# Kernel optimization log

Measured on AMD Instinct MI355X. Metric: run time of the kernel, lower is better.

Reference implementation:

```python
import jax, jax.numpy as jnp
import numpy as np

N1, N2, C, H = 512, 512, 256, 512

def setup_inputs() -> dict:
    key = jax.random.key(0)
    ks = jax.random.split(key, 8)
    std = 0.01
    return {
        "X": jax.random.normal(ks[0], (N1, C), dtype=jnp.float32),
        "Y": jax.random.normal(ks[1], (N2, C), dtype=jnp.float32),
        "W_sr": jax.random.normal(ks[2], (C, C), dtype=jnp.float32) * std,   # project_sr.weight
        "W_tg": jax.random.normal(ks[3], (C, C), dtype=jnp.float32) * std,   # project_tg.weight
        "W1": jax.random.normal(ks[4], (H, 2 * C), dtype=jnp.float32) * std, # fc_M[0].weight [512,512]
        "b1": jnp.zeros((H,), dtype=jnp.float32),                            # fc_M[0].bias
        "w2": jax.random.normal(ks[5], (1, H), dtype=jnp.float32) * std,     # fc_M[2].weight [1,512]
        "b2": jnp.zeros((1,), dtype=jnp.float32),                            # fc_M[2].bias
    }

def reference(X, Y, W_sr, W_tg, W1, b1, w2, b2):
    # Projections (Linear without bias): x @ W.T
    Xp = X @ W_sr.T  # [N1, C]
    Yp = Y @ W_tg.T  # [N2, C]
    # fc_M first layer acts on concat([X_k, Y_k], -1); split W1 into the
    # halves that multiply Xp and Yp respectively (mathematically identical
    # to materializing the [N1,N2,2C] concat, but avoids it).
    W1x, W1y = W1[:, :C], W1[:, C:]
    hx = Xp @ W1x.T                     # [N1, H]
    hy = Yp @ W1y.T                     # [N2, H]
    Hid = jax.nn.relu(hx[:, None, :] + hy[None, :, :] + b1)  # [N1, N2, H]
    M = Hid @ w2[0] + b2[0]             # [N1, N2]  (squeeze of last dim 1)
    return M
```

## Files before the change

### kernel.cpp

```cpp
#include <hip/hip_runtime.h>


typedef _Float16 h2 __attribute__((ext_vector_type(2)));
typedef _Float16 h4 __attribute__((ext_vector_type(4)));
typedef _Float16 h8 __attribute__((ext_vector_type(8)));

__global__ __launch_bounds__(128) void gemm1_f16(
    const float* __restrict__ A0, const float* __restrict__ A1,
    const float* __restrict__ B0, const float* __restrict__ B1,
    _Float16* __restrict__ C0, _Float16* __restrict__ C1,
    const float* __restrict__ b2, float* __restrict__ out)
{
    const int z = blockIdx.z;
    const float* A = z ? A1 : A0;
    const float* B = z ? B1 : B0;
    _Float16* Cc   = z ? C1 : C0;

    __shared__ _Float16 As2[16 * 72];
    __shared__ _Float16 Bs2[16 * 72];

    const int t  = threadIdx.x;
    const int m0 = blockIdx.x * 32;
    const int n0 = blockIdx.y * 32;
    const int ti = t >> 4;
    const int tj = t & 15;

    {
        const int bid = blockIdx.x + 16 * (blockIdx.y + 8 * blockIdx.z);
        const float bb = b2[0];
        float4 f = {bb, bb, bb, bb};
        float* o = out + bid * 1024 + t * 8;
        *(float4*)o = f;
        *(float4*)(o + 4) = f;
    }

    float acc[4][2] = {};

    float4 va[2], vb[2];
    #pragma unroll
    for (int r = 0; r < 2; r++) {
        const int id = t + r * 128;
        va[r] = *(const float4*)&A[(m0 + (id >> 3)) * 256 + (id & 7) * 4];
        vb[r] = *(const float4*)&B[(n0 + (id >> 3)) * 256 + (id & 7) * 4];
    }

    for (int kt = 0; kt < 256; kt += 32) {
        #pragma unroll
        for (int r = 0; r < 2; r++) {
            const int id  = t + r * 128;
            const int m   = id >> 3;
            const int k4  = (id & 7) * 4;
            const int kp0 = k4 >> 1;
            h2 alo = {(_Float16)va[r].x, (_Float16)va[r].y};
            h2 ahi = {(_Float16)va[r].z, (_Float16)va[r].w};
            *(h2*)&As2[kp0 * 72 + 2 * m]       = alo;
            *(h2*)&As2[(kp0 + 1) * 72 + 2 * m] = ahi;
            h2 blo = {(_Float16)vb[r].x, (_Float16)vb[r].y};
            h2 bhi = {(_Float16)vb[r].z, (_Float16)vb[r].w};
            *(h2*)&Bs2[kp0 * 72 + 2 * m]       = blo;
            *(h2*)&Bs2[(kp0 + 1) * 72 + 2 * m] = bhi;
        }
        __syncthreads();

        if (kt < 224) {
            #pragma unroll
            for (int r = 0; r < 2; r++) {
                const int id = t + r * 128;
                va[r] = *(const float4*)&A[(m0 + (id >> 3)) * 256 + kt + 32 + (id & 7) * 4];
                vb[r] = *(const float4*)&B[(n0 + (id >> 3)) * 256 + kt + 32 + (id & 7) * 4];
            }
        }

        #pragma unroll 8
        for (int kp = 0; kp < 16; kp++) {
            h8 a = *(const h8*)&As2[kp * 72 + 8 * ti];
            h4 b = *(const h4*)&Bs2[kp * 72 + 4 * tj];
            const h2* ap = (const h2*)&a;
            const h2* bp = (const h2*)&b;
            #pragma unroll
            for (int mi = 0; mi < 4; mi++)
                #pragma unroll
                for (int nj = 0; nj < 2; nj++)
                    acc[mi][nj] = __builtin_amdgcn_fdot2(ap[mi], bp[nj],
                                                         acc[mi][nj], false);
        }
        __syncthreads();
    }

    #pragma unroll
    for (int mi = 0; mi < 4; mi++) {
        const int m = m0 + 4 * ti + mi;
        h2 r = {(_Float16)acc[mi][0], (_Float16)acc[mi][1]};
        *(h2*)&Cc[m * 256 + n0 + 2 * tj] = r;
    }
}

__global__ __launch_bounds__(128) void gemm2_f16(
    const _Float16* __restrict__ A0, const _Float16* __restrict__ A1,
    const float* __restrict__ B0, const float* __restrict__ B1,
    _Float16* __restrict__ C0, _Float16* __restrict__ C1,
    const float* __restrict__ bias1)
{
    const int z = blockIdx.z;
    const _Float16* A = z ? A1 : A0;
    const float* B    = z ? B1 : B0;
    _Float16* Cc      = z ? C1 : C0;
    const float* bias = z ? bias1 : nullptr;

    __shared__ _Float16 As2[16 * 72];
    __shared__ _Float16 Bs2[16 * 136];

    const int t  = threadIdx.x;
    const int m0 = blockIdx.x * 32;
    const int n0 = blockIdx.y * 64;
    const int ti = t >> 4;
    const int tj = t & 15;

    float acc[4][4] = {};

    h8 va;
    float4 vb[4];
    {
        const int m  = t >> 2;
        const int k8 = (t & 3) * 8;
        va = *(const h8*)&A[(m0 + m) * 256 + k8];
    }
    #pragma unroll
    for (int r = 0; r < 4; r++) {
        const int id = t + r * 128;
        vb[r] = *(const float4*)&B[(n0 + (id >> 3)) * 512 + (id & 7) * 4];
    }

    for (int kt = 0; kt < 256; kt += 32) {
        {
            const int m   = t >> 2;
            const int k8  = (t & 3) * 8;
            const int kp0 = k8 >> 1;
            #pragma unroll
            for (int i = 0; i < 4; i++) {
                h2 p = {va[2 * i], va[2 * i + 1]};
                *(h2*)&As2[(kp0 + i) * 72 + 2 * m] = p;
            }
        }
        #pragma unroll
        for (int r = 0; r < 4; r++) {
            const int id  = t + r * 128;
            const int n   = id >> 3;
            const int k4  = (id & 7) * 4;
            const int kp0 = k4 >> 1;
            h2 lo = {(_Float16)vb[r].x, (_Float16)vb[r].y};
            h2 hi = {(_Float16)vb[r].z, (_Float16)vb[r].w};
            *(h2*)&Bs2[kp0 * 136 + 2 * n]       = lo;
            *(h2*)&Bs2[(kp0 + 1) * 136 + 2 * n] = hi;
        }
        __syncthreads();

        if (kt < 224) {
            const int m  = t >> 2;
            const int k8 = (t & 3) * 8;
            va = *(const h8*)&A[(m0 + m) * 256 + kt + 32 + k8];
            #pragma unroll
            for (int r = 0; r < 4; r++) {
                const int id = t + r * 128;
                vb[r] = *(const float4*)&B[(n0 + (id >> 3)) * 512 + kt + 32 + (id & 7) * 4];
            }
        }

        #pragma unroll 8
        for (int kp = 0; kp < 16; kp++) {
            h8 a = *(const h8*)&As2[kp * 72 + 8 * ti];
            h8 b = *(const h8*)&Bs2[kp * 136 + 8 * tj];
            const h2* ap = (const h2*)&a;
            const h2* bp = (const h2*)&b;
            #pragma unroll
            for (int mi = 0; mi < 4; mi++)
                #pragma unroll
                for (int nj = 0; nj < 4; nj++)
                    acc[mi][nj] = __builtin_amdgcn_fdot2(ap[mi], bp[nj],
                                                         acc[mi][nj], false);
        }
        __syncthreads();
    }

    float4 bv = {0.f, 0.f, 0.f, 0.f};
    if (bias) bv = *(const float4*)&bias[n0 + 4 * tj];
    #pragma unroll
    for (int mi = 0; mi < 4; mi++) {
        const int m = m0 + 4 * ti + mi;
        h4 r = {(_Float16)(acc[mi][0] + bv.x), (_Float16)(acc[mi][1] + bv.y),
                (_Float16)(acc[mi][2] + bv.z), (_Float16)(acc[mi][3] + bv.w)};
        *(h4*)&Cc[m * 512 + n0 + 4 * tj] = r;
    }
}

__global__ __launch_bounds__(256) void affinity_core(
    const _Float16* __restrict__ hx, const _Float16* __restrict__ hy,
    const float* __restrict__ w2, float* __restrict__ out)
{
    __shared__ __align__(16) _Float16 xs[64 * 72];
    __shared__ __align__(16) _Float16 ys[64 * 72];
    __shared__ __align__(16) _Float16 ws2[64];

    const int t  = threadIdx.x;
    const int i0 = blockIdx.x * 64;
    const int j0 = blockIdx.y * 64;
    const int h0 = blockIdx.z * 64;
    const int ti = t / 16;
    const int tj = t % 16;

    #pragma unroll
    for (int s = 0; s < 2; s++) {
        const int id = t + s * 256;
        const int r  = id >> 3;
        const int c8 = (id & 7) * 8;
        *(float4*)&xs[r * 72 + c8] = *(const float4*)&hx[(i0 + r) * 512 + h0 + c8];
        *(float4*)&ys[r * 72 + c8] = *(const float4*)&hy[(j0 + r) * 512 + h0 + c8];
    }
    if (t < 64) ws2[t] = (_Float16)w2[h0 + t];
    __syncthreads();

    float acc[4][4] = {};
    const _Float16* xr = xs + ti * 72;
    const _Float16* yr = ys + tj * 72;
    const h2 hz = {(_Float16)0.f, (_Float16)0.f};

    #pragma unroll 2
    for (int g = 0; g < 8; g++) {
        const int ho = g * 8;
        h8 w = *(const h8*)&ws2[ho];
        h8 x[4], y[4];
        #pragma unroll
        for (int m = 0; m < 4; m++) x[m] = *(const h8*)&xr[m * (16 * 72) + ho];
        #pragma unroll
        for (int n = 0; n < 4; n++) y[n] = *(const h8*)&yr[n * (16 * 72) + ho];
        const h2* wp = (const h2*)&w;
        #pragma unroll
        for (int m = 0; m < 4; m++) {
            const h2* xp = (const h2*)&x[m];
            #pragma unroll
            for (int n = 0; n < 4; n++) {
                const h2* yp = (const h2*)&y[n];
                float a = acc[m][n];
                #pragma unroll
                for (int p = 0; p < 4; p++) {
                    h2 s = xp[p] + yp[p];
                    s = __builtin_elementwise_max(s, hz);
                    a = __builtin_amdgcn_fdot2(s, wp[p], a, false);
                }
                acc[m][n] = a;
            }
        }
    }

    #pragma unroll
    for (int m = 0; m < 4; m++) {
        #pragma unroll
        for (int n = 0; n < 4; n++) {
            atomicAdd(&out[(i0 + ti + 16 * m) * 512 + (j0 + tj + 16 * n)],
                      acc[m][n]);
        }
    }
}

extern "C" void kernel_launch(void* const* d_in, const int* in_sizes, int n_in,
                              void* d_out, int out_size, void* d_ws, size_t ws_size,
                              hipStream_t stream) {
    const float* X    = (const float*)d_in[0];
    const float* Y    = (const float*)d_in[1];
    const float* W_sr = (const float*)d_in[2];
    const float* W_tg = (const float*)d_in[3];
    const float* W1   = (const float*)d_in[4];
    const float* b1   = (const float*)d_in[5];
    const float* w2   = (const float*)d_in[6];
    const float* b2   = (const float*)d_in[7];

    float* ws = (float*)d_ws;
    _Float16* Xp = (_Float16*)ws;
    _Float16* Yp = (_Float16*)(ws + 65536);
    _Float16* hx = (_Float16*)(ws + 131072);
    _Float16* hy = (_Float16*)(ws + 262144);
    float* out = (float*)d_out;

    gemm1_f16<<<dim3(16, 8, 2), 128, 0, stream>>>(
        X, Y, W_sr, W_tg, Xp, Yp, b2, out);
    gemm2_f16<<<dim3(16, 8, 2), 128, 0, stream>>>(
        Xp, Yp, W1, W1 + 256, hx, hy, b1);
    affinity_core<<<dim3(8, 8, 8), 256, 0, stream>>>(hx, hy, w2, out);
}
```

Baseline: 98.58 us.

## Load full K panel into shared memory once in both projection GEMMs

```diff
diff --git a/kernel.cpp b/kernel.cpp
--- a/kernel.cpp
+++ b/kernel.cpp
@@ -16,8 +16,8 @@
     const float* B = z ? B1 : B0;
     _Float16* Cc   = z ? C1 : C0;
 
-    __shared__ _Float16 As2[16 * 72];
-    __shared__ _Float16 Bs2[16 * 72];
+    __shared__ _Float16 As2[128 * 72];
+    __shared__ _Float16 Bs2[128 * 72];
 
     const int t  = threadIdx.x;
     const int m0 = blockIdx.x * 32;
@@ -34,57 +34,42 @@
         *(float4*)(o + 4) = f;
     }
 
-    float acc[4][2] = {};
-
-    float4 va[2], vb[2];
-    #pragma unroll
-    for (int r = 0; r < 2; r++) {
-        const int id = t + r * 128;
-        va[r] = *(const float4*)&A[(m0 + (id >> 3)) * 256 + (id & 7) * 4];
-        vb[r] = *(const float4*)&B[(n0 + (id >> 3)) * 256 + (id & 7) * 4];
-    }
-
-    for (int kt = 0; kt < 256; kt += 32) {
-        #pragma unroll
-        for (int r = 0; r < 2; r++) {
-            const int id  = t + r * 128;
+    #pragma unroll 4
+    for (int r = 0; r < 8; r++) {
+        const int kt = r * 32;
+        #pragma unroll
+        for (int s = 0; s < 2; s++) {
+            const int id  = t + s * 128;
             const int m   = id >> 3;
             const int k4  = (id & 7) * 4;
-            const int kp0 = k4 >> 1;
-            h2 alo = {(_Float16)va[r].x, (_Float16)va[r].y};
-            h2 ahi = {(_Float16)va[r].z, (_Float16)va[r].w};
+            const int kp0 = r * 16 + (k4 >> 1);
+            float4 va = *(const float4*)&A[(m0 + m) * 256 + kt + k4];
+            h2 alo = {(_Float16)va.x, (_Float16)va.y};
+            h2 ahi = {(_Float16)va.z, (_Float16)va.w};
             *(h2*)&As2[kp0 * 72 + 2 * m]       = alo;
             *(h2*)&As2[(kp0 + 1) * 72 + 2 * m] = ahi;
-            h2 blo = {(_Float16)vb[r].x, (_Float16)vb[r].y};
-            h2 bhi = {(_Float16)vb[r].z, (_Float16)vb[r].w};
+            float4 vb = *(const float4*)&B[(n0 + m) * 256 + kt + k4];
+            h2 blo = {(_Float16)vb.x, (_Float16)vb.y};
+            h2 bhi = {(_Float16)vb.z, (_Float16)vb.w};
             *(h2*)&Bs2[kp0 * 72 + 2 * m]       = blo;
             *(h2*)&Bs2[(kp0 + 1) * 72 + 2 * m] = bhi;
         }
-        __syncthreads();
-
-        if (kt < 224) {
-            #pragma unroll
-            for (int r = 0; r < 2; r++) {
-                const int id = t + r * 128;
-                va[r] = *(const float4*)&A[(m0 + (id >> 3)) * 256 + kt + 32 + (id & 7) * 4];
-                vb[r] = *(const float4*)&B[(n0 + (id >> 3)) * 256 + kt + 32 + (id & 7) * 4];
-            }
-        }
-
-        #pragma unroll 8
-        for (int kp = 0; kp < 16; kp++) {
-            h8 a = *(const h8*)&As2[kp * 72 + 8 * ti];
-            h4 b = *(const h4*)&Bs2[kp * 72 + 4 * tj];
-            const h2* ap = (const h2*)&a;
-            const h2* bp = (const h2*)&b;
-            #pragma unroll
-            for (int mi = 0; mi < 4; mi++)
-                #pragma unroll
-                for (int nj = 0; nj < 2; nj++)
-                    acc[mi][nj] = __builtin_amdgcn_fdot2(ap[mi], bp[nj],
-                                                         acc[mi][nj], false);
-        }
-        __syncthreads();
+    }
+    __syncthreads();
+
+    float acc[4][2] = {};
+    #pragma unroll 8
+    for (int kp = 0; kp < 128; kp++) {
+        h8 a = *(const h8*)&As2[kp * 72 + 8 * ti];
+        h4 b = *(const h4*)&Bs2[kp * 72 + 4 * tj];
+        const h2* ap = (const h2*)&a;
+        const h2* bp = (const h2*)&b;
+        #pragma unroll
+        for (int mi = 0; mi < 4; mi++)
+            #pragma unroll
+            for (int nj = 0; nj < 2; nj++)
+                acc[mi][nj] = __builtin_amdgcn_fdot2(ap[mi], bp[nj],
+                                                     acc[mi][nj], false);
     }
 
     #pragma unroll
@@ -107,8 +92,8 @@
     _Float16* Cc      = z ? C1 : C0;
     const float* bias = z ? bias1 : nullptr;
 
-    __shared__ _Float16 As2[16 * 72];
-    __shared__ _Float16 Bs2[16 * 136];
+    __shared__ _Float16 As2[128 * 72];
+    __shared__ _Float16 Bs2[128 * 136];
 
     const int t  = threadIdx.x;
     const int m0 = blockIdx.x * 32;
@@ -116,70 +101,48 @@
     const int ti = t >> 4;
     const int tj = t & 15;
 
-    float acc[4][4] = {};
-
-    h8 va;
-    float4 vb[4];
-    {
-        const int m  = t >> 2;
-        const int k8 = (t & 3) * 8;
-        va = *(const h8*)&A[(m0 + m) * 256 + k8];
-    }
-    #pragma unroll
-    for (int r = 0; r < 4; r++) {
-        const int id = t + r * 128;
-        vb[r] = *(const float4*)&B[(n0 + (id >> 3)) * 512 + (id & 7) * 4];
-    }
-
-    for (int kt = 0; kt < 256; kt += 32) {
+    #pragma unroll 4
+    for (int r = 0; r < 8; r++) {
+        const int kt = r * 32;
         {
             const int m   = t >> 2;
             const int k8  = (t & 3) * 8;
-            const int kp0 = k8 >> 1;
+            const int kp0 = r * 16 + (k8 >> 1);
+            h8 v = *(const h8*)&A[(m0 + m) * 256 + kt + k8];
             #pragma unroll
             for (int i = 0; i < 4; i++) {
-                h2 p = {va[2 * i], va[2 * i + 1]};
+                h2 p = {v[2 * i], v[2 * i + 1]};
                 *(h2*)&As2[(kp0 + i) * 72 + 2 * m] = p;
             }
         }
         #pragma unroll
-        for (int r = 0; r < 4; r++) {
-            const int id  = t + r * 128;
+        for (int s = 0; s < 4; s++) {
+            const int id  = t + s * 128;
             const int n   = id >> 3;
             const int k4  = (id & 7) * 4;
-            const int kp0 = k4 >> 1;
-            h2 lo = {(_Float16)vb[r].x, (_Float16)vb[r].y};
-            h2 hi = {(_Float16)vb[r].z, (_Float16)vb[r].w};
+            const int kp0 = r * 16 + (k4 >> 1);
+            float4 v = *(const float4*)&B[(n0 + n) * 512 + kt + k4];
+            h2 lo = {(_Float16)v.x, (_Float16)v.y};
+            h2 hi = {(_Float16)v.z, (_Float16)v.w};
             *(h2*)&Bs2[kp0 * 136 + 2 * n]       = lo;
             *(h2*)&Bs2[(kp0 + 1) * 136 + 2 * n] = hi;
         }
-        __syncthreads();
-
-        if (kt < 224) {
-            const int m  = t >> 2;
-            const int k8 = (t & 3) * 8;
-            va = *(const h8*)&A[(m0 + m) * 256 + kt + 32 + k8];
-            #pragma unroll
-            for (int r = 0; r < 4; r++) {
-                const int id = t + r * 128;
-                vb[r] = *(const float4*)&B[(n0 + (id >> 3)) * 512 + kt + 32 + (id & 7) * 4];
-            }
-        }
-
-        #pragma unroll 8
-        for (int kp = 0; kp < 16; kp++) {
-            h8 a = *(const h8*)&As2[kp * 72 + 8 * ti];
-            h8 b = *(const h8*)&Bs2[kp * 136 + 8 * tj];
-            const h2* ap = (const h2*)&a;
-            const h2* bp = (const h2*)&b;
-            #pragma unroll
-            for (int mi = 0; mi < 4; mi++)
-                #pragma unroll
-                for (int nj = 0; nj < 4; nj++)
-                    acc[mi][nj] = __builtin_amdgcn_fdot2(ap[mi], bp[nj],
-                                                         acc[mi][nj], false);
-        }
-        __syncthreads();
+    }
+    __syncthreads();
+
+    float acc[4][4] = {};
+    #pragma unroll 8
+    for (int kp = 0; kp < 128; kp++) {
+        h8 a = *(const h8*)&As2[kp * 72 + 8 * ti];
+        h8 b = *(const h8*)&Bs2[kp * 136 + 8 * tj];
+        const h2* ap = (const h2*)&a;
+        const h2* bp = (const h2*)&b;
+        #pragma unroll
+        for (int mi = 0; mi < 4; mi++)
+            #pragma unroll
+            for (int nj = 0; nj < 4; nj++)
+                acc[mi][nj] = __builtin_amdgcn_fdot2(ap[mi], bp[nj],
+                                                     acc[mi][nj], false);
     }
 
     float4 bv = {0.f, 0.f, 0.f, 0.f};
```

After: 95.12 us, median of 2. 1.04x faster.
